# Kernel tuning notes

Hardware: AMD Instinct MI355X
Metric: run time of the kernel (lower is better)

## Reference

```python
import jax, jax.numpy as jnp
import numpy as np

VOCAB = 50000
D = 256          # vector_dim == hidden size
SEQ = 128
BATCH = 4096
NUM_CLASSES = 5


def setup_inputs() -> dict:
    key = jax.random.key(0)
    ks = jax.random.split(key, 8)
    x = jax.random.randint(ks[0], (BATCH, SEQ), 0, VOCAB, dtype=jnp.int64)
    scale = 1.0 / np.sqrt(D)
    emb = jax.random.normal(ks[1], (VOCAB, D), dtype=jnp.float32)
    emb = emb.at[0].set(0.0)  # padding_idx=0 row is zero
    W_ih = jax.random.uniform(ks[2], (D, D), jnp.float32, -scale, scale)
    W_hh = jax.random.uniform(ks[3], (D, D), jnp.float32, -scale, scale)
    b_ih = jax.random.uniform(ks[4], (D,), jnp.float32, -scale, scale)
    b_hh = jax.random.uniform(ks[5], (D,), jnp.float32, -scale, scale)
    W_cls = jax.random.uniform(ks[6], (NUM_CLASSES, D), jnp.float32, -scale, scale)
    b_cls = jax.random.uniform(ks[7], (NUM_CLASSES,), jnp.float32, -scale, scale)
    return {"x": x, "emb": emb, "W_ih": W_ih, "W_hh": W_hh,
            "b_ih": b_ih, "b_hh": b_hh, "W_cls": W_cls, "b_cls": b_cls}


def reference(x, emb, W_ih, W_hh, b_ih, b_hh, W_cls, b_cls):
    # Embedding lookup: [B, S, D]
    xe = emb[x]
    # Precompute input projections for all timesteps in one GEMM.
    x_proj = jnp.einsum("bsd,hd->bsh", xe, W_ih) + b_ih + b_hh  # [B, S, D]

    def step(h, xp_t):
        h = jnp.tanh(xp_t + h @ W_hh.T)
        return h, None

    h0 = jnp.zeros((x.shape[0], W_hh.shape[0]), dtype=xe.dtype)
    # scan over time axis: [S, B, D]
    h_last, _ = jax.lax.scan(step, h0, jnp.swapaxes(x_proj, 0, 1))
    # classifier on last step
    return h_last @ W_cls.T + b_cls  # [B, 5]
```

## Files before the change

### kernel.cpp

```cpp
#include <hip/hip_runtime.h>


typedef __attribute__((ext_vector_type(8))) short bf16x8;
typedef __attribute__((ext_vector_type(4))) float f32x4;

#define LDS_STRIDE 264
#define VOCAB 50000
#define NBLK_EMB 768

__device__ __align__(256) unsigned short g_P[VOCAB * 256];

static __device__ __forceinline__ float bf2f(unsigned short u) {
    union { unsigned int i; float f; } v; v.i = ((unsigned int)u) << 16; return v.f;
}
static __device__ __forceinline__ unsigned short f2bf(float f) {
    union { float f; unsigned int i; } v; v.f = f;
    unsigned int r = v.i + 0x7FFFu + ((v.i >> 16) & 1u);
    return (unsigned short)(r >> 16);
}
static __device__ __forceinline__ bf16x8 cvt8(float4 a, float4 b) {
    bf16x8 r;
    r[0] = (short)f2bf(a.x); r[1] = (short)f2bf(a.y);
    r[2] = (short)f2bf(a.z); r[3] = (short)f2bf(a.w);
    r[4] = (short)f2bf(b.x); r[5] = (short)f2bf(b.y);
    r[6] = (short)f2bf(b.z); r[7] = (short)f2bf(b.w);
    return r;
}
static __device__ __forceinline__ bf16x8 load8_bf(const float* __restrict__ p) {
    return cvt8(((const float4*)p)[0], ((const float4*)p)[1]);
}
static __device__ __forceinline__ float fast_tanh(float x) {
    x = fminf(8.f, fmaxf(-8.f, x));
    float e = __expf(2.f * x);
    return 1.f - 2.f * __builtin_amdgcn_rcpf(e + 1.f);
}

__global__ __launch_bounds__(256)
void emb_proj_kernel(const float* __restrict__ emb,
                     const float* __restrict__ W_ih,
                     const float* __restrict__ b_ih,
                     const float* __restrict__ b_hh)
{
    __shared__ __align__(16) unsigned short tin [16 * LDS_STRIDE];
    __shared__ __align__(16) unsigned short tout[16 * LDS_STRIDE];
    const int tid  = threadIdx.x;
    const int lane = tid & 63;
    const int wid  = tid >> 6;
    const int n0   = wid * 64;
    const int row  = tid >> 4, seg = tid & 15;

    bf16x8 wf[4][8];
    float  bias[4];
    #pragma unroll
    for (int nt = 0; nt < 4; ++nt) {
        int n = n0 + nt * 16 + (lane & 15);
        bias[nt] = b_ih[n] + b_hh[n];
        #pragma unroll
        for (int kt = 0; kt < 8; ++kt)
            wf[nt][kt] = load8_bf(W_ih + n * 256 + (lane >> 4) * 8 + kt * 32);
    }

    int tile = blockIdx.x;
    float4 a0, a1, a2, a3;
    {
        const float4* s = (const float4*)(emb + ((size_t)tile * 16 + row) * 256 + seg * 16);
        a0 = s[0]; a1 = s[1]; a2 = s[2]; a3 = s[3];
    }

    for (; tile < 3125; tile += NBLK_EMB) {
        *(bf16x8*)(&tin[row * LDS_STRIDE + seg * 16])     = cvt8(a0, a1);
        *(bf16x8*)(&tin[row * LDS_STRIDE + seg * 16 + 8]) = cvt8(a2, a3);
        int tn = tile + NBLK_EMB;
        if (tn < 3125) {
            const float4* s = (const float4*)(emb + ((size_t)tn * 16 + row) * 256 + seg * 16);
            a0 = s[0]; a1 = s[1]; a2 = s[2]; a3 = s[3];
        }
        __syncthreads();

        f32x4 acc[4];
        #pragma unroll
        for (int nt = 0; nt < 4; ++nt) acc[nt] = (f32x4){0.f, 0.f, 0.f, 0.f};
        #pragma unroll
        for (int kt = 0; kt < 8; ++kt) {
            bf16x8 a = *(bf16x8*)(&tin[(lane & 15) * LDS_STRIDE + (lane >> 4) * 8 + kt * 32]);
            #pragma unroll
            for (int nt = 0; nt < 4; ++nt)
                acc[nt] = __builtin_amdgcn_mfma_f32_16x16x32_bf16(a, wf[nt][kt], acc[nt], 0, 0, 0);
        }
        #pragma unroll
        for (int nt = 0; nt < 4; ++nt) {
            int n = n0 + nt * 16 + (lane & 15);
            #pragma unroll
            for (int r = 0; r < 4; ++r)
                tout[((lane >> 4) * 4 + r) * LDS_STRIDE + n] = f2bf(acc[nt][r] + bias[nt]);
        }
        __syncthreads();
        {
            uint4 o0 = *(uint4*)(&tout[row * LDS_STRIDE + seg * 16]);
            uint4 o1 = *(uint4*)(&tout[row * LDS_STRIDE + seg * 16 + 8]);
            uint4* dst = (uint4*)(g_P + ((size_t)tile * 16 + row) * 256 + seg * 16);
            dst[0] = o0; dst[1] = o1;
        }
    }
}

__global__ __launch_bounds__(512, 1)
void rnn_kernel(const int* __restrict__ x,
                const float* __restrict__ W_hh,
                const float* __restrict__ W_cls,
                const float* __restrict__ b_cls,
                float* __restrict__ out)
{
    __shared__ __align__(16) unsigned short h_lds [2][16 * LDS_STRIDE];
    __shared__ __align__(16) unsigned short xp_lds[2][16 * LDS_STRIDE];
    __shared__ __align__(16) int tok_lds[16 * 128];
    __shared__ __align__(16) float wcls_lds[5 * 256];
    __shared__ float bcls_lds[5];

    const int tid   = threadIdx.x;
    const int lane  = tid & 63;
    const int wid   = tid >> 6;
    const int b0    = blockIdx.x * 16;
    const int n0    = wid * 32;
    const int grow  = tid >> 5;
    const int gseg  = tid & 31;

    bf16x8 wf[2][8];
    #pragma unroll
    for (int nt = 0; nt < 2; ++nt) {
        int n = n0 + nt * 16 + (lane & 15);
        #pragma unroll
        for (int kt = 0; kt < 8; ++kt)
            wf[nt][kt] = load8_bf(W_hh + n * 256 + (lane >> 4) * 8 + kt * 32);
    }

    ((int4*)tok_lds)[tid] = ((const int4*)(x + (size_t)b0 * 128))[tid];
    if (tid < 320) ((float4*)wcls_lds)[tid] = ((const float4*)W_cls)[tid];
    if (tid < 5)   bcls_lds[tid] = b_cls[tid];
    for (int i = tid; i < 16 * LDS_STRIDE / 2; i += 512) ((unsigned int*)h_lds[0])[i] = 0;

    float4 p_cur;
    {
        int t0 = x[(size_t)(b0 + grow) * 128 + 0];
        t0 = min(max(t0, 0), VOCAB - 1);
        *(float4*)(&xp_lds[0][grow * LDS_STRIDE + gseg * 8]) =
            *(const float4*)(g_P + (size_t)t0 * 256 + gseg * 8);
        int t1 = x[(size_t)(b0 + grow) * 128 + 1];
        t1 = min(max(t1, 0), VOCAB - 1);
        p_cur = *(const float4*)(g_P + (size_t)t1 * 256 + gseg * 8);
    }
    __syncthreads();

    const int colA = (lane & 15) * LDS_STRIDE + (lane >> 4) * 8;
    const int colC = ((lane >> 4) * 4) * LDS_STRIDE + n0 + (lane & 15);
    const unsigned short* hA0 = &h_lds[0][colA];
    const unsigned short* hA1 = &h_lds[1][colA];
    const unsigned short* xR0 = &xp_lds[0][colC];
    const unsigned short* xR1 = &xp_lds[1][colC];
    unsigned short* hW0 = &h_lds[0][colC];
    unsigned short* hW1 = &h_lds[1][colC];
    unsigned short* gw0 = &xp_lds[0][grow * LDS_STRIDE + gseg * 8];
    unsigned short* gw1 = &xp_lds[1][grow * LDS_STRIDE + gseg * 8];

    auto step = [&](const unsigned short* hA, const unsigned short* xR,
                    unsigned short* hW, unsigned short* gw, int t) {
        float4 p_nxt;
        if (t + 2 < 128) {
            int tok = tok_lds[grow * 128 + t + 2];
            tok = min(max(tok, 0), VOCAB - 1);
            p_nxt = *(const float4*)(g_P + (size_t)tok * 256 + gseg * 8);
        }
        float xp[2][4];
        #pragma unroll
        for (int nt = 0; nt < 2; ++nt)
            #pragma unroll
            for (int r = 0; r < 4; ++r)
                xp[nt][r] = bf2f(xR[r * LDS_STRIDE + nt * 16]);
        f32x4 acc0 = (f32x4){0.f, 0.f, 0.f, 0.f};
        f32x4 acc1 = (f32x4){0.f, 0.f, 0.f, 0.f};
        #pragma unroll
        for (int kt = 0; kt < 8; ++kt) {
            bf16x8 a = *(const bf16x8*)(hA + kt * 32);
            acc0 = __builtin_amdgcn_mfma_f32_16x16x32_bf16(a, wf[0][kt], acc0, 0, 0, 0);
            acc1 = __builtin_amdgcn_mfma_f32_16x16x32_bf16(a, wf[1][kt], acc1, 0, 0, 0);
        }
        #pragma unroll
        for (int r = 0; r < 4; ++r) {
            hW[r * LDS_STRIDE]      = f2bf(fast_tanh(acc0[r] + xp[0][r]));
            hW[r * LDS_STRIDE + 16] = f2bf(fast_tanh(acc1[r] + xp[1][r]));
        }
        if (t + 1 < 128)
            *(float4*)gw = p_cur;
        p_cur = p_nxt;
    };

    #pragma unroll 1
    for (int t2 = 0; t2 < 64; ++t2) {
        step(hA0, xR0, hW1, gw1, 2 * t2);
        __syncthreads();
        step(hA1, xR1, hW0, gw0, 2 * t2 + 1);
        __syncthreads();
    }

    if (tid < 80) {
        int row = tid / 5, c = tid % 5;
        float acc = bcls_lds[c];
        for (int k = 0; k < 256; ++k)
            acc += bf2f(h_lds[0][row * LDS_STRIDE + k]) * wcls_lds[c * 256 + k];
        out[(size_t)(b0 + row) * 5 + c] = acc;
    }
}

extern "C" void kernel_launch(void* const* d_in, const int* in_sizes, int n_in,
                              void* d_out, int out_size, void* d_ws, size_t ws_size,
                              hipStream_t stream)
{
    const int*   x     = (const int*)d_in[0];
    const float* emb   = (const float*)d_in[1];
    const float* W_ih  = (const float*)d_in[2];
    const float* W_hh  = (const float*)d_in[3];
    const float* b_ih  = (const float*)d_in[4];
    const float* b_hh  = (const float*)d_in[5];
    const float* W_cls = (const float*)d_in[6];
    const float* b_cls = (const float*)d_in[7];
    float*       out   = (float*)d_out;
    (void)d_ws; (void)ws_size;

    emb_proj_kernel<<<NBLK_EMB, 256, 0, stream>>>(emb, W_ih, b_ih, b_hh);
    rnn_kernel<<<256, 512, 0, stream>>>(x, W_hh, W_cls, b_cls, out);
}
```

Before: 241.0 us.

## Gather projections directly into MFMA accumulators and swizzle hidden-state LDS layout

The RNN kernel now gathers the precomputed input projections straight from global memory in the MFMA C-fragment layout and uses them as the initial accumulator values. This removes the xp LDS staging buffer and its extra read and write each step. The hidden-state LDS buffer uses an XOR swizzle instead of padding, and tokens are stored transposed. Other changes: two blocks per CU are requested, tanh and bf16 rounding are cheaper, token clamping is dropped, the classifier is spread over more threads with shuffles, and the embedding grid is reduced. The narrower scattered 2-byte global gathers on the step-critical path may add latency, and the faster rounding changes numerics slightly.

```diff
diff --git a/kernel.cpp b/kernel.cpp
--- a/kernel.cpp
+++ b/kernel.cpp
@@ -4,35 +4,42 @@
 typedef __attribute__((ext_vector_type(8))) short bf16x8;
 typedef __attribute__((ext_vector_type(4))) float f32x4;
 
+#define VOCAB 50000
+#define NBLK_EMB 256
 #define LDS_STRIDE 264
-#define VOCAB 50000
-#define NBLK_EMB 768
 
 __device__ __align__(256) unsigned short g_P[VOCAB * 256];
 
 static __device__ __forceinline__ float bf2f(unsigned short u) {
     union { unsigned int i; float f; } v; v.i = ((unsigned int)u) << 16; return v.f;
 }
-static __device__ __forceinline__ unsigned short f2bf(float f) {
+static __device__ __forceinline__ float bfbits2f(unsigned int zext_u16) {
+    union { unsigned int i; float f; } v; v.i = zext_u16 << 16; return v.f;
+}
+static __device__ __forceinline__ unsigned short f2bf_rne(float f) {
     union { float f; unsigned int i; } v; v.f = f;
     unsigned int r = v.i + 0x7FFFu + ((v.i >> 16) & 1u);
     return (unsigned short)(r >> 16);
 }
+static __device__ __forceinline__ unsigned short f2bf_fast(float f) {
+    union { float f; unsigned int i; } v; v.f = f;
+    return (unsigned short)((v.i + 0x8000u) >> 16);
+}
 static __device__ __forceinline__ bf16x8 cvt8(float4 a, float4 b) {
     bf16x8 r;
-    r[0] = (short)f2bf(a.x); r[1] = (short)f2bf(a.y);
-    r[2] = (short)f2bf(a.z); r[3] = (short)f2bf(a.w);
-    r[4] = (short)f2bf(b.x); r[5] = (short)f2bf(b.y);
-    r[6] = (short)f2bf(b.z); r[7] = (short)f2bf(b.w);
+    r[0] = (short)f2bf_rne(a.x); r[1] = (short)f2bf_rne(a.y);
+    r[2] = (short)f2bf_rne(a.z); r[3] = (short)f2bf_rne(a.w);
+    r[4] = (short)f2bf_rne(b.x); r[5] = (short)f2bf_rne(b.y);
+    r[6] = (short)f2bf_rne(b.z); r[7] = (short)f2bf_rne(b.w);
     return r;
 }
 static __device__ __forceinline__ bf16x8 load8_bf(const float* __restrict__ p) {
     return cvt8(((const float4*)p)[0], ((const float4*)p)[1]);
 }
 static __device__ __forceinline__ float fast_tanh(float x) {
-    x = fminf(8.f, fmaxf(-8.f, x));
+    x = __builtin_amdgcn_fmed3f(x, -8.f, 8.f);
     float e = __expf(2.f * x);
-    return 1.f - 2.f * __builtin_amdgcn_rcpf(e + 1.f);
+    return __builtin_fmaf(-2.f, __builtin_amdgcn_rcpf(e + 1.f), 1.f);
 }
 
 __global__ __launch_bounds__(256)
@@ -92,7 +99,7 @@
             int n = n0 + nt * 16 + (lane & 15);
             #pragma unroll
             for (int r = 0; r < 4; ++r)
-                tout[((lane >> 4) * 4 + r) * LDS_STRIDE + n] = f2bf(acc[nt][r] + bias[nt]);
+                tout[((lane >> 4) * 4 + r) * LDS_STRIDE + n] = f2bf_rne(acc[nt][r] + bias[nt]);
         }
         __syncthreads();
         {
@@ -104,110 +111,125 @@
     }
 }
 
-__global__ __launch_bounds__(512, 1)
+__global__ __launch_bounds__(512, 2)
 void rnn_kernel(const int* __restrict__ x,
                 const float* __restrict__ W_hh,
                 const float* __restrict__ W_cls,
                 const float* __restrict__ b_cls,
                 float* __restrict__ out)
 {
-    __shared__ __align__(16) unsigned short h_lds [2][16 * LDS_STRIDE];
-    __shared__ __align__(16) unsigned short xp_lds[2][16 * LDS_STRIDE];
-    __shared__ __align__(16) int tok_lds[16 * 128];
+    __shared__ __align__(16) unsigned short h_lds[2][16 * 256];
+    __shared__ __align__(16) int tok_t[128 * 16];
     __shared__ __align__(16) float wcls_lds[5 * 256];
     __shared__ float bcls_lds[5];
 
-    const int tid   = threadIdx.x;
-    const int lane  = tid & 63;
-    const int wid   = tid >> 6;
-    const int b0    = blockIdx.x * 16;
-    const int n0    = wid * 32;
-    const int grow  = tid >> 5;
-    const int gseg  = tid & 31;
+    const int tid  = threadIdx.x;
+    const int lane = tid & 63;
+    const int wid  = tid >> 6;
+    const int b0   = blockIdx.x * 16;
+    const int n0   = wid * 32;
+    const int l15  = lane & 15;
+    const int quad = lane >> 4;
 
     bf16x8 wf[2][8];
     #pragma unroll
     for (int nt = 0; nt < 2; ++nt) {
-        int n = n0 + nt * 16 + (lane & 15);
+        int n = n0 + nt * 16 + l15;
         #pragma unroll
         for (int kt = 0; kt < 8; ++kt)
-            wf[nt][kt] = load8_bf(W_hh + n * 256 + (lane >> 4) * 8 + kt * 32);
-    }
-
-    ((int4*)tok_lds)[tid] = ((const int4*)(x + (size_t)b0 * 128))[tid];
+            wf[nt][kt] = load8_bf(W_hh + n * 256 + quad * 8 + kt * 32);
+    }
+
+    {
+        int row = tid & 15, tq = tid >> 4;
+        int4 v = *(const int4*)(x + (size_t)(b0 + row) * 128 + tq * 4);
+        tok_t[(tq * 4 + 0) * 16 + row] = v.x;
+        tok_t[(tq * 4 + 1) * 16 + row] = v.y;
+        tok_t[(tq * 4 + 2) * 16 + row] = v.z;
+        tok_t[(tq * 4 + 3) * 16 + row] = v.w;
+    }
     if (tid < 320) ((float4*)wcls_lds)[tid] = ((const float4*)W_cls)[tid];
     if (tid < 5)   bcls_lds[tid] = b_cls[tid];
-    for (int i = tid; i < 16 * LDS_STRIDE / 2; i += 512) ((unsigned int*)h_lds[0])[i] = 0;
-
-    float4 p_cur;
-    {
-        int t0 = x[(size_t)(b0 + grow) * 128 + 0];
-        t0 = min(max(t0, 0), VOCAB - 1);
-        *(float4*)(&xp_lds[0][grow * LDS_STRIDE + gseg * 8]) =
-            *(const float4*)(g_P + (size_t)t0 * 256 + gseg * 8);
-        int t1 = x[(size_t)(b0 + grow) * 128 + 1];
-        t1 = min(max(t1, 0), VOCAB - 1);
-        p_cur = *(const float4*)(g_P + (size_t)t1 * 256 + gseg * 8);
+    #pragma unroll
+    for (int i = 0; i < 4; ++i) ((unsigned int*)h_lds[0])[tid + i * 512] = 0;
+
+    int aoff[8];
+    #pragma unroll
+    for (int kt = 0; kt < 8; ++kt)
+        aoff[kt] = l15 * 512 + (((quad + 4 * kt) ^ l15) << 4);
+    int woff[8];
+    #pragma unroll
+    for (int nt = 0; nt < 2; ++nt)
+        #pragma unroll
+        for (int r = 0; r < 4; ++r) {
+            int row = quad * 4 + r;
+            int g   = (n0 >> 3) + nt * 2 + (l15 >> 3);
+            woff[nt * 4 + r] = row * 512 + ((g ^ row) << 4) + (l15 & 7) * 2;
+        }
+
+    const unsigned int colByte = (unsigned int)(n0 + l15) * 2;
+
+    unsigned int gA[8], gB[8];
+    #pragma unroll
+    for (int r = 0; r < 4; ++r) {
+        const int* xr = x + (size_t)(b0 + quad * 4 + r) * 128;
+        const unsigned short* p0 = g_P + (size_t)xr[0] * 256 + n0 + l15;
+        const unsigned short* p1 = g_P + (size_t)xr[1] * 256 + n0 + l15;
+        gA[r] = p0[0]; gA[4 + r] = p0[16];
+        gB[r] = p1[0]; gB[4 + r] = p1[16];
     }
     __syncthreads();
 
-    const int colA = (lane & 15) * LDS_STRIDE + (lane >> 4) * 8;
-    const int colC = ((lane >> 4) * 4) * LDS_STRIDE + n0 + (lane & 15);
-    const unsigned short* hA0 = &h_lds[0][colA];
-    const unsigned short* hA1 = &h_lds[1][colA];
-    const unsigned short* xR0 = &xp_lds[0][colC];
-    const unsigned short* xR1 = &xp_lds[1][colC];
-    unsigned short* hW0 = &h_lds[0][colC];
-    unsigned short* hW1 = &h_lds[1][colC];
-    unsigned short* gw0 = &xp_lds[0][grow * LDS_STRIDE + gseg * 8];
-    unsigned short* gw1 = &xp_lds[1][grow * LDS_STRIDE + gseg * 8];
-
-    auto step = [&](const unsigned short* hA, const unsigned short* xR,
-                    unsigned short* hW, unsigned short* gw, int t) {
-        float4 p_nxt;
+    char* const h0 = (char*)&h_lds[0][0];
+
+    auto step = [&](const char* hA, char* hW, unsigned int* g, int t) {
+        f32x4 acc0 = { bfbits2f(g[0]), bfbits2f(g[1]), bfbits2f(g[2]), bfbits2f(g[3]) };
+        f32x4 acc1 = { bfbits2f(g[4]), bfbits2f(g[5]), bfbits2f(g[6]), bfbits2f(g[7]) };
         if (t + 2 < 128) {
-            int tok = tok_lds[grow * 128 + t + 2];
-            tok = min(max(tok, 0), VOCAB - 1);
-            p_nxt = *(const float4*)(g_P + (size_t)tok * 256 + gseg * 8);
-        }
-        float xp[2][4];
-        #pragma unroll
-        for (int nt = 0; nt < 2; ++nt)
-            #pragma unroll
-            for (int r = 0; r < 4; ++r)
-                xp[nt][r] = bf2f(xR[r * LDS_STRIDE + nt * 16]);
-        f32x4 acc0 = (f32x4){0.f, 0.f, 0.f, 0.f};
-        f32x4 acc1 = (f32x4){0.f, 0.f, 0.f, 0.f};
+            int4 tk = *(const int4*)&tok_t[(t + 2) * 16 + quad * 4];
+            const unsigned short* r0 = (const unsigned short*)((const char*)g_P + ((unsigned int)tk.x * 512 + colByte));
+            const unsigned short* r1 = (const unsigned short*)((const char*)g_P + ((unsigned int)tk.y * 512 + colByte));
+            const unsigned short* r2 = (const unsigned short*)((const char*)g_P + ((unsigned int)tk.z * 512 + colByte));
+            const unsigned short* r3 = (const unsigned short*)((const char*)g_P + ((unsigned int)tk.w * 512 + colByte));
+            g[0] = r0[0]; g[4] = r0[16];
+            g[1] = r1[0]; g[5] = r1[16];
+            g[2] = r2[0]; g[6] = r2[16];
+            g[3] = r3[0]; g[7] = r3[16];
+        }
         #pragma unroll
         for (int kt = 0; kt < 8; ++kt) {
-            bf16x8 a = *(const bf16x8*)(hA + kt * 32);
+            bf16x8 a = *(const bf16x8*)(hA + aoff[kt]);
             acc0 = __builtin_amdgcn_mfma_f32_16x16x32_bf16(a, wf[0][kt], acc0, 0, 0, 0);
             acc1 = __builtin_amdgcn_mfma_f32_16x16x32_bf16(a, wf[1][kt], acc1, 0, 0, 0);
         }
         #pragma unroll
         for (int r = 0; r < 4; ++r) {
-            hW[r * LDS_STRIDE]      = f2bf(fast_tanh(acc0[r] + xp[0][r]));
-            hW[r * LDS_STRIDE + 16] = f2bf(fast_tanh(acc1[r] + xp[1][r]));
-        }
-        if (t + 1 < 128)
-            *(float4*)gw = p_cur;
-        p_cur = p_nxt;
+            *(unsigned short*)(hW + woff[r])     = f2bf_fast(fast_tanh(acc0[r]));
+            *(unsigned short*)(hW + woff[4 + r]) = f2bf_fast(fast_tanh(acc1[r]));
+        }
     };
 
     #pragma unroll 1
     for (int t2 = 0; t2 < 64; ++t2) {
-        step(hA0, xR0, hW1, gw1, 2 * t2);
-        __syncthreads();
-        step(hA1, xR1, hW0, gw0, 2 * t2 + 1);
-        __syncthreads();
-    }
-
-    if (tid < 80) {
-        int row = tid / 5, c = tid % 5;
-        float acc = bcls_lds[c];
-        for (int k = 0; k < 256; ++k)
-            acc += bf2f(h_lds[0][row * LDS_STRIDE + k]) * wcls_lds[c * 256 + k];
-        out[(size_t)(b0 + row) * 5 + c] = acc;
+        step(h0,        h0 + 8192, gA, 2 * t2);
+        __syncthreads();
+        step(h0 + 8192, h0,        gB, 2 * t2 + 1);
+        __syncthreads();
+    }
+
+    if (tid < 320) {
+        int q = tid & 3, p = tid >> 2;
+        int row = p / 5, c = p - row * 5;
+        float acc = 0.f;
+        #pragma unroll
+        for (int kk = 0; kk < 64; ++kk) {
+            int k = q * 64 + kk;
+            int off = row * 512 + ((((k >> 3) ^ row)) << 4) + (k & 7) * 2;
+            acc += bf2f(*(const unsigned short*)(h0 + off)) * wcls_lds[c * 256 + k];
+        }
+        acc += __shfl_xor(acc, 1);
+        acc += __shfl_xor(acc, 2);
+        if (q == 0) out[(size_t)(b0 + row) * 5 + c] = acc + bcls_lds[c];
     }
 }
 
```

Result: faster. 226.1 us (-6.2%).
